# Kernel optimization log

Measured on AMD Instinct MI355X. Metric: run time of the kernel, lower is better.

The kernel has to match this reference:

```python
import jax, jax.numpy as jnp
import numpy as np

N_NODES = 100000
N_EDGES = 3200000
IN_DIM = 256
HID_DIM = 64
OUT_DIM = 64


def setup_inputs() -> dict:
    key = jax.random.key(0)
    k1, k2, k3, k4, k5, k6 = jax.random.split(key, 6)
    x = jax.random.normal(k1, (N_NODES, IN_DIM), dtype=jnp.float32)
    edge_index = jax.random.randint(k2, (2, N_EDGES), 0, N_NODES, dtype=jnp.int32)
    # Glorot-style init for the two GCNConv layers (PyG default: glorot weight, zero bias)
    W1 = jax.random.normal(k3, (IN_DIM, HID_DIM), dtype=jnp.float32) * (1.0 / np.sqrt(IN_DIM))
    b1 = jnp.zeros((HID_DIM,), dtype=jnp.float32)
    W2 = jax.random.normal(k4, (HID_DIM, OUT_DIM), dtype=jnp.float32) * (1.0 / np.sqrt(HID_DIM))
    b2 = jnp.zeros((OUT_DIM,), dtype=jnp.float32)
    return {"x": x, "edge_index": edge_index, "W1": W1, "b1": b1, "W2": W2, "b2": b2}


def _gcn_conv(x, src, dst, deg_inv_sqrt, W, b, n):
    # PyG GCNConv: h = x W; out_i = sum_j norm_ij * h_j + b, with symmetric norm
    h = x @ W                                   # (n, d_out) small GEMM
    norm = deg_inv_sqrt[src] * deg_inv_sqrt[dst]  # (E+n,)
    msg = norm[:, None] * h[src]                # gather (E+n, d_out)
    agg = jax.ops.segment_sum(msg, dst, num_segments=n)  # scatter-add
    return agg + b


def reference(x, edge_index, W1, b1, W2, b2):
    n = x.shape[0]
    loops = jnp.arange(n, dtype=edge_index.dtype)
    src = jnp.concatenate([edge_index[0], loops])
    dst = jnp.concatenate([edge_index[1], loops])
    # degree on destination (col) with added self-loops, weight 1.0
    deg = jax.ops.segment_sum(jnp.ones_like(dst, dtype=x.dtype), dst, num_segments=n)
    deg_inv_sqrt = jnp.where(deg > 0, jax.lax.rsqrt(deg), 0.0)
    h = jax.nn.relu(_gcn_conv(x, src, dst, deg_inv_sqrt, W1, b1, n))
    return _gcn_conv(h, src, dst, deg_inv_sqrt, W2, b2, n)
```

## Files before the change

kernel.cpp:

```cpp
#include <hip/hip_runtime.h>
#include <cstdint>
#include <cstddef>


#define BIN_SHIFT 7
#define BIN_NODES 128
#define MAX_BINS 1024
#define SUP_SHIFT 11
#define FINE_PER_SUP 16
#define NSUP_MAX 64
#define SCAP 56
#define SRC_BITS 17
#define SRC_MASK ((1 << SRC_BITS) - 1)

typedef unsigned short ushort_t;

typedef __attribute__((ext_vector_type(8))) short bf16x8;
typedef __attribute__((ext_vector_type(4))) float f32x4;

union FragB {
  uint4 u;
  bf16x8 b;
};

__device__ __forceinline__ float4 bfq2f4(uint2 p) {
  float4 r;
  r.x = __uint_as_float(p.x << 16);
  r.y = __uint_as_float(p.x & 0xFFFF0000u);
  r.z = __uint_as_float(p.y << 16);
  r.w = __uint_as_float(p.y & 0xFFFF0000u);
  return r;
}
__device__ __forceinline__ unsigned f2bf(float f) {
  unsigned u = __float_as_uint(f);
  return (u + 0x7FFFu + ((u >> 16) & 1u)) >> 16;
}
__device__ __forceinline__ uint2 f42bfq(float4 f) {
  uint2 r;
  r.x = f2bf(f.x) | (f2bf(f.y) << 16);
  r.y = f2bf(f.z) | (f2bf(f.w) << 16);
  return r;
}

__global__ void zero_int(int* __restrict__ p, int n) {
  int i = blockIdx.x * blockDim.x + threadIdx.x;
  if (i < n) p[i] = 0;
}

__global__ __launch_bounds__(256) void bin_count(const int* __restrict__ dst, int E, int nbins,
                                                 int* __restrict__ binCnt) {
  __shared__ int h[MAX_BINS];
  for (int i = threadIdx.x; i < nbins; i += 256) h[i] = 0;
  __syncthreads();
  int stride = gridDim.x * 256;
  for (int e = blockIdx.x * 256 + threadIdx.x; e < E; e += stride)
    atomicAdd(&h[dst[e] >> BIN_SHIFT], 1);
  __syncthreads();
  for (int i = threadIdx.x; i < nbins; i += 256)
    if (h[i]) atomicAdd(&binCnt[i], h[i]);
}

__global__ __launch_bounds__(256) void bin_scan(const int* __restrict__ binCnt, int nbins, int E,
                                                int* __restrict__ binStart,
                                                int* __restrict__ binCursor,
                                                int* __restrict__ supCursor) {
  __shared__ int s[256];
  int t = threadIdx.x;
  int c[4];
  int sum = 0;
#pragma unroll
  for (int i = 0; i < 4; i++) {
    int idx = t * 4 + i;
    c[i] = (idx < nbins) ? binCnt[idx] : 0;
    sum += c[i];
  }
  int v = sum;
  s[t] = v;
  __syncthreads();
  for (int d = 1; d < 256; d <<= 1) {
    int add = (t >= d) ? s[t - d] : 0;
    __syncthreads();
    s[t] += add;
    __syncthreads();
  }
  int run = s[t] - v;
#pragma unroll
  for (int i = 0; i < 4; i++) {
    int idx = t * 4 + i;
    if (idx < nbins) {
      binStart[idx] = run;
      binCursor[idx] = run;
      if ((idx & (FINE_PER_SUP - 1)) == 0) supCursor[idx >> 4] = run;
      run += c[i];
    }
  }
  if (t == 0) binStart[nbins] = E;
}

__global__ __launch_bounds__(256) void super_fill(const int* __restrict__ src,
                                                  const int* __restrict__ dst, int E, int nsup,
                                                  int* __restrict__ supCursor,
                                                  unsigned* __restrict__ supbuf) {
  __shared__ unsigned stage[NSUP_MAX * SCAP];
  __shared__ int lcnt[NSUP_MAX], lbase[NSUP_MAX], lscan[NSUP_MAX + 1];
  const int tid = threadIdx.x;
  const int t0 = blockIdx.x * 2048;
  const int t1 = min(E, t0 + 2048);

  int dv[8], sv[8];
#pragma unroll
  for (int i = 0; i < 8; i++) {
    int e = t0 + i * 256 + tid;
    if (e < t1) {
      dv[i] = dst[e];
      sv[i] = src[e];
    }
  }
  if (tid < nsup) lcnt[tid] = 0;
  __syncthreads();
#pragma unroll
  for (int i = 0; i < 8; i++) {
    int e = t0 + i * 256 + tid;
    if (e < t1) {
      int d = dv[i];
      int sb = d >> SUP_SHIFT;
      unsigned v = ((unsigned)(d & ((1 << SUP_SHIFT) - 1)) << SRC_BITS) | (unsigned)sv[i];
      int idx = atomicAdd(&lcnt[sb], 1);
      if (idx < SCAP)
        stage[sb * SCAP + idx] = v;
      else {
        int g = atomicAdd(&supCursor[sb], 1);
        supbuf[g] = v;
      }
    }
  }
  __syncthreads();
  if (tid < nsup) {
    int c = min(lcnt[tid], SCAP);
    lcnt[tid] = c;
    lbase[tid] = c ? atomicAdd(&supCursor[tid], c) : 0;
  }
  __syncthreads();
  if (tid < 64) {
    int vv = (tid < nsup) ? lcnt[tid] : 0;
    int ss = vv;
#pragma unroll
    for (int d = 1; d < 64; d <<= 1) {
      int u = __shfl_up(ss, d);
      if (tid >= d) ss += u;
    }
    lscan[tid + 1] = ss;
    if (tid == 0) lscan[0] = 0;
  }
  __syncthreads();
  int total = lscan[nsup];
  for (int j = tid; j < total; j += 256) {
    int lo = 0, hi = nsup;
    while (hi - lo > 1) {
      int mid = (lo + hi) >> 1;
      if (lscan[mid] <= j)
        lo = mid;
      else
        hi = mid;
    }
    int off = j - lscan[lo];
    supbuf[lbase[lo] + off] = stage[lo * SCAP + off];
  }
}

__global__ __launch_bounds__(256) void fine_fill(const unsigned* __restrict__ supbuf,
                                                 const int* __restrict__ binStart, int nbins,
                                                 int* __restrict__ binCursor,
                                                 unsigned* __restrict__ binbuf) {
  __shared__ int lcnt[FINE_PER_SUP], lbase[FINE_PER_SUP];
  int sb = blockIdx.x >> 3, p = blockIdx.x & 7;
  int seg0 = binStart[sb << 4];
  int seg1 = binStart[min((sb + 1) << 4, nbins)];
  int part = (seg1 - seg0 + 7) >> 3;
  int c0 = seg0 + p * part;
  int c1 = min(seg1, c0 + part);
  if (threadIdx.x < FINE_PER_SUP) lcnt[threadIdx.x] = 0;
  __syncthreads();
  for (int i = c0 + threadIdx.x; i < c1; i += 256) atomicAdd(&lcnt[supbuf[i] >> 24], 1);
  __syncthreads();
  if (threadIdx.x < FINE_PER_SUP) {
    int c = lcnt[threadIdx.x];
    lbase[threadIdx.x] = c ? atomicAdd(&binCursor[(sb << 4) + threadIdx.x], c) : 0;
    lcnt[threadIdx.x] = 0;
  }
  __syncthreads();
  for (int i = c0 + threadIdx.x; i < c1; i += 256) {
    unsigned v = supbuf[i];
    unsigned dls = v >> SRC_BITS;
    int f = dls >> BIN_SHIFT;
    unsigned vf = ((dls & (BIN_NODES - 1)) << SRC_BITS) | (v & SRC_MASK);
    int idx = lbase[f] + atomicAdd(&lcnt[f], 1);
    binbuf[idx] = vf;
  }
}

__global__ __launch_bounds__(256) void node_count_dis(const unsigned* __restrict__ binbuf,
                                                      const int* __restrict__ binStart, int N,
                                                      int* __restrict__ count,
                                                      float* __restrict__ dis) {
  __shared__ int cnt[BIN_NODES];
  int b = blockIdx.x;
  int nodeBase = b << BIN_SHIFT;
  if (threadIdx.x < BIN_NODES) cnt[threadIdx.x] = 0;
  __syncthreads();
  int s0 = binStart[b], s1 = binStart[b + 1];
  for (int i = s0 + threadIdx.x; i < s1; i += 256) atomicAdd(&cnt[binbuf[i] >> SRC_BITS], 1);
  __syncthreads();
  if (threadIdx.x < BIN_NODES) {
    int node = nodeBase + threadIdx.x;
    if (node < N) {
      int c = cnt[threadIdx.x];
      count[node] = c;
      dis[node] = rsqrtf((float)(c + 1));
    }
  }
}

__global__ __launch_bounds__(256) void bin_csr(const unsigned* __restrict__ binbuf,
                                               const int* __restrict__ binStart,
                                               const int* __restrict__ count, int N, int E,
                                               int* __restrict__ rowptr, int* __restrict__ col) {
  __shared__ int cur[BIN_NODES];
  __shared__ int pref[BIN_NODES];
  int b = blockIdx.x, t = threadIdx.x;
  int nodeBase = b << BIN_SHIFT;
  int c = 0;
  if (t < BIN_NODES) {
    int node = nodeBase + t;
    c = (node < N) ? count[node] : 0;
    pref[t] = c;
  }
  __syncthreads();
  for (int d = 1; d < BIN_NODES; d <<= 1) {
    int add = (t < BIN_NODES && t >= d) ? pref[t - d] : 0;
    __syncthreads();
    if (t < BIN_NODES) pref[t] += add;
    __syncthreads();
  }
  int s0 = binStart[b];
  if (t < BIN_NODES) {
    int node = nodeBase + t;
    if (node < N) {
      int ex = s0 + pref[t] - c;
      rowptr[node] = ex;
      cur[t] = ex;
    }
  }
  if (b == 0 && t == 255) rowptr[N] = E;
  __syncthreads();
  int s1 = binStart[b + 1];
  for (int i = s0 + t; i < s1; i += 256) {
    unsigned v = binbuf[i];
    int slot = atomicAdd(&cur[v >> SRC_BITS], 1);
    col[slot] = v & SRC_MASK;
  }
}

__global__ __launch_bounds__(256) void wsplit(const float* __restrict__ W1,
                                              const float* __restrict__ W2,
                                              ushort_t* __restrict__ wt1,
                                              ushort_t* __restrict__ wt2) {
  int i = blockIdx.x * 256 + threadIdx.x;
  const float* W;
  ushort_t* wt;
  int K, idx;
  if (i < 256 * 64) {
    W = W1; wt = wt1; K = 256; idx = i;
  } else if (i < 256 * 64 + 64 * 64) {
    W = W2; wt = wt2; K = 64; idx = i - 256 * 64;
  } else
    return;
  int n = idx & 63, k = idx >> 6;
  float f = W[k * 64 + n];
  unsigned u = __float_as_uint(f);
  unsigned hb = u & 0xFFFF0000u;
  float lo = f - __uint_as_float(hb);
  wt[(size_t)n * K + k] = (ushort_t)(u >> 16);
  wt[(size_t)64 * K + (size_t)n * K + k] = (ushort_t)(__float_as_uint(lo) >> 16);
}

__device__ __forceinline__ void split8u(uint4 a, uint4 b, uint4& xh, uint4& xl) {
  unsigned ua[8] = {a.x, a.y, a.z, a.w, b.x, b.y, b.z, b.w};
  unsigned hw[4], lw[4];
#pragma unroll
  for (int p = 0; p < 4; p++) {
    unsigned u0 = ua[2 * p], u1 = ua[2 * p + 1];
    unsigned h0 = u0 & 0xFFFF0000u, h1 = u1 & 0xFFFF0000u;
    float l0 = __uint_as_float(u0) - __uint_as_float(h0);
    float l1 = __uint_as_float(u1) - __uint_as_float(h1);
    hw[p] = (u0 >> 16) | h1;
    lw[p] = (__float_as_uint(l0) >> 16) | (__float_as_uint(l1) & 0xFFFF0000u);
  }
  xh = make_uint4(hw[0], hw[1], hw[2], hw[3]);
  xl = make_uint4(lw[0], lw[1], lw[2], lw[3]);
}

__global__ __launch_bounds__(256, 3) void gemm1_mfma(const float* __restrict__ A,
                                                     const ushort_t* __restrict__ Wt,
                                                     uint2* __restrict__ Cb, int M) {
  constexpr int K = 256;
  __shared__ uint4 xtile[3][4][256];
  const int lane = threadIdx.x & 63;
  const int wv = threadIdx.x >> 6;
  const int l15 = lane & 15;
  const int lq = lane >> 4;
  const int m0 = blockIdx.x * 128 + wv * 32;

  const ushort_t* __restrict__ Wlo = Wt + (size_t)64 * K;

  f32x4 acc[2][4];
#pragma unroll
  for (int a = 0; a < 2; a++)
#pragma unroll
    for (int b = 0; b < 4; b++) acc[a][b] = (f32x4){0.f, 0.f, 0.f, 0.f};

  auto stage_tile = [&](int kt, int buf) {
#pragma unroll
    for (int c = 0; c < 4; c++) {
      int s = c * 64 + lane;
      int r = s >> 3;
      int c4 = (s & 7) ^ (r & 7);
      int nd = m0 + r;
      if (nd >= M) nd = M - 1;
      const float* gp = A + (size_t)nd * K + kt * 32 + c4 * 4;
      __builtin_amdgcn_global_load_lds(
          (const __attribute__((address_space(1))) void*)gp,
          (__attribute__((address_space(3))) void*)&xtile[buf][wv][c * 64], 16, 0, 0);
    }
  };

  stage_tile(0, 0);
  stage_tile(1, 1);
  __builtin_amdgcn_sched_barrier(0);

#pragma unroll
  for (int j = 0; j < 8; j++) {
    if (j < 7)
      asm volatile("s_waitcnt vmcnt(4)" ::: "memory");
    else
      asm volatile("s_waitcnt vmcnt(0)" ::: "memory");
    __builtin_amdgcn_sched_barrier(0);
    FragB w[8];
    {
      const int kb = j * 32 + lq * 8;
#pragma unroll
      for (int nt = 0; nt < 4; nt++) {
        w[nt].u = *(const uint4*)(Wt + (size_t)(nt * 16 + l15) * K + kb);
        w[4 + nt].u = *(const uint4*)(Wlo + (size_t)(nt * 16 + l15) * K + kb);
      }
    }
    uint4 xa[2][2];
#pragma unroll
    for (int mt = 0; mt < 2; mt++) {
      int mr = mt * 16 + l15;
#pragma unroll
      for (int hh = 0; hh < 2; hh++) {
        int c4 = (lq * 2 + hh) ^ (mr & 7);
        xa[mt][hh] = *(const uint4*)&xtile[j % 3][wv][mr * 8 + c4];
      }
    }
    __builtin_amdgcn_sched_barrier(0);
    if (j + 2 < 8) stage_tile(j + 2, (j + 2) % 3);
    __builtin_amdgcn_sched_barrier(0);
    FragB xh0, xl0, xh1, xl1;
    split8u(xa[0][0], xa[0][1], xh0.u, xl0.u);
    split8u(xa[1][0], xa[1][1], xh1.u, xl1.u);
#pragma unroll
    for (int nt = 0; nt < 4; nt++) {
      acc[0][nt] = __builtin_amdgcn_mfma_f32_16x16x32_bf16(w[nt].b, xh0.b, acc[0][nt], 0, 0, 0);
      acc[0][nt] = __builtin_amdgcn_mfma_f32_16x16x32_bf16(w[nt].b, xl0.b, acc[0][nt], 0, 0, 0);
      acc[1][nt] = __builtin_amdgcn_mfma_f32_16x16x32_bf16(w[nt].b, xh1.b, acc[1][nt], 0, 0, 0);
      acc[1][nt] = __builtin_amdgcn_mfma_f32_16x16x32_bf16(w[nt].b, xl1.b, acc[1][nt], 0, 0, 0);
    }
#pragma unroll
    for (int nt = 0; nt < 4; nt++) {
      acc[0][nt] = __builtin_amdgcn_mfma_f32_16x16x32_bf16(w[4 + nt].b, xh0.b, acc[0][nt], 0, 0, 0);
      acc[1][nt] = __builtin_amdgcn_mfma_f32_16x16x32_bf16(w[4 + nt].b, xh1.b, acc[1][nt], 0, 0, 0);
    }
  }

#pragma unroll
  for (int mt = 0; mt < 2; mt++) {
    int node = m0 + mt * 16 + l15;
    if (node < M) {
      uint2* cp = Cb + (size_t)node * 16 + lq;
#pragma unroll
      for (int nt = 0; nt < 4; nt++) {
        float4 o = make_float4(acc[mt][nt][0], acc[mt][nt][1], acc[mt][nt][2], acc[mt][nt][3]);
        cp[nt * 4] = f42bfq(o);
      }
    }
  }
}

__global__ __launch_bounds__(256, 3) void gemm2_mfma(const ushort_t* __restrict__ Av,
                                                     const ushort_t* __restrict__ Wt,
                                                     uint2* __restrict__ Cb, int M) {
  constexpr int K = 64;
  constexpr int NT = K / 32;
  const int lane = threadIdx.x & 63;
  const int wv = threadIdx.x >> 6;
  const int l15 = lane & 15;
  const int lq = lane >> 4;
  const int m0 = blockIdx.x * 128 + wv * 32;

  const ushort_t* __restrict__ Wlo = Wt + (size_t)64 * K;

  f32x4 acc[2][4];
#pragma unroll
  for (int a = 0; a < 2; a++)
#pragma unroll
    for (int b = 0; b < 4; b++) acc[a][b] = (f32x4){0.f, 0.f, 0.f, 0.f};

  int node[2], ncl[2];
#pragma unroll
  for (int mt = 0; mt < 2; mt++) {
    node[mt] = m0 + mt * 16 + l15;
    ncl[mt] = node[mt] < M ? node[mt] : (M - 1);
  }

  FragB xa[NT][2], wh[NT][4], wl[NT][4];
#pragma unroll
  for (int t = 0; t < NT; t++)
#pragma unroll
    for (int mt = 0; mt < 2; mt++)
      xa[t][mt].u = *(const uint4*)(Av + (size_t)ncl[mt] * K + t * 32 + lq * 8);
#pragma unroll
  for (int t = 0; t < NT; t++)
#pragma unroll
    for (int nt = 0; nt < 4; nt++) {
      wh[t][nt].u = *(const uint4*)(Wt + (size_t)(nt * 16 + l15) * K + t * 32 + lq * 8);
      wl[t][nt].u = *(const uint4*)(Wlo + (size_t)(nt * 16 + l15) * K + t * 32 + lq * 8);
    }
#pragma unroll
  for (int t = 0; t < NT; t++)
#pragma unroll
    for (int mt = 0; mt < 2; mt++)
#pragma unroll
      for (int nt = 0; nt < 4; nt++) {
        acc[mt][nt] =
            __builtin_amdgcn_mfma_f32_16x16x32_bf16(wh[t][nt].b, xa[t][mt].b, acc[mt][nt], 0, 0, 0);
        acc[mt][nt] =
            __builtin_amdgcn_mfma_f32_16x16x32_bf16(wl[t][nt].b, xa[t][mt].b, acc[mt][nt], 0, 0, 0);
      }

#pragma unroll
  for (int mt = 0; mt < 2; mt++) {
    if (node[mt] < M) {
      uint2* cp = Cb + (size_t)node[mt] * 16 + lq;
#pragma unroll
      for (int nt = 0; nt < 4; nt++) {
        float4 o = make_float4(acc[mt][nt][0], acc[mt][nt][1], acc[mt][nt][2], acc[mt][nt][3]);
        cp[nt * 4] = f42bfq(o);
      }
    }
  }
}

template <bool OUTBF>
__global__ __launch_bounds__(256) void agg_kernel(
    const uint2* __restrict__ h, const int* __restrict__ rowptr, const int* __restrict__ col,
    const float* __restrict__ dis, const float* __restrict__ bias, void* __restrict__ outv,
    int N, int relu) {
  int wq = (blockIdx.x * blockDim.x + threadIdx.x) >> 6;
  int n0 = wq * 4;
  if (n0 >= N) return;
  int lane = threadIdx.x & 63;
  int sub = lane & 15;
  int quarter = lane >> 4;

  int rp[5];
  float dd[4];
#pragma unroll
  for (int i = 0; i < 5; i++) rp[i] = rowptr[min(n0 + i, N)];
#pragma unroll
  for (int i = 0; i < 4; i++) dd[i] = (n0 + i < N) ? dis[n0 + i] : 0.f;
  float4 bv = ((const float4*)bias)[sub];

#pragma unroll
  for (int ni = 0; ni < 4; ni++) {
    int wid = n0 + ni;
    if (wid >= N) break;
    int start = rp[ni], end = rp[ni + 1];
    float di = dd[ni];

    float4 a0 = make_float4(0.f, 0.f, 0.f, 0.f), a1 = a0, a2 = a0, a3 = a0;
    {
      float4 self = bfq2f4(h[(size_t)wid * 16 + sub]);
      if (quarter == 0) {
        a0.x = di * self.x;
        a0.y = di * self.y;
        a0.z = di * self.z;
        a0.w = di * self.w;
      }
    }

    for (int base = start; base < end; base += 64) {
      int e = base + lane;
      int sj = 0;
      float wj = 0.f;
      if (e < end) {
        sj = col[e];
        wj = dis[sj];
      }
      int cnt = end - base;
      if (cnt > 64) cnt = 64;
      int rounds = (cnt + 3) >> 2;
      int t = 0;
      for (; t + 4 <= rounds; t += 4) {
        int i0 = 4 * t + quarter;
        int s0 = __shfl(sj, i0), s1 = __shfl(sj, i0 + 4), s2 = __shfl(sj, i0 + 8),
            s3 = __shfl(sj, i0 + 12);
        float w0 = __shfl(wj, i0), w1 = __shfl(wj, i0 + 4), w2 = __shfl(wj, i0 + 8),
              w3 = __shfl(wj, i0 + 12);
        float4 g0 = bfq2f4(h[(size_t)s0 * 16 + sub]);
        float4 g1 = bfq2f4(h[(size_t)s1 * 16 + sub]);
        float4 g2 = bfq2f4(h[(size_t)s2 * 16 + sub]);
        float4 g3 = bfq2f4(h[(size_t)s3 * 16 + sub]);
        a0.x += w0 * g0.x; a0.y += w0 * g0.y; a0.z += w0 * g0.z; a0.w += w0 * g0.w;
        a1.x += w1 * g1.x; a1.y += w1 * g1.y; a1.z += w1 * g1.z; a1.w += w1 * g1.w;
        a2.x += w2 * g2.x; a2.y += w2 * g2.y; a2.z += w2 * g2.z; a2.w += w2 * g2.w;
        a3.x += w3 * g3.x; a3.y += w3 * g3.y; a3.z += w3 * g3.z; a3.w += w3 * g3.w;
      }
      for (; t < rounds; t++) {
        int i0 = 4 * t + quarter;
        int s0 = __shfl(sj, i0);
        float w0 = __shfl(wj, i0);
        float4 g0 = bfq2f4(h[(size_t)s0 * 16 + sub]);
        a0.x += w0 * g0.x; a0.y += w0 * g0.y; a0.z += w0 * g0.z; a0.w += w0 * g0.w;
      }
    }

    float sx = (a0.x + a1.x) + (a2.x + a3.x);
    float sy = (a0.y + a1.y) + (a2.y + a3.y);
    float sz = (a0.z + a1.z) + (a2.z + a3.z);
    float sw = (a0.w + a1.w) + (a2.w + a3.w);
    sx += __shfl_down(sx, 32); sy += __shfl_down(sy, 32);
    sz += __shfl_down(sz, 32); sw += __shfl_down(sw, 32);
    sx += __shfl_down(sx, 16); sy += __shfl_down(sy, 16);
    sz += __shfl_down(sz, 16); sw += __shfl_down(sw, 16);
    if (quarter == 0) {
      float4 o = make_float4(di * sx + bv.x, di * sy + bv.y, di * sz + bv.z, di * sw + bv.w);
      if (relu) {
        o.x = fmaxf(o.x, 0.f);
        o.y = fmaxf(o.y, 0.f);
        o.z = fmaxf(o.z, 0.f);
        o.w = fmaxf(o.w, 0.f);
      }
      if (OUTBF)
        ((uint2*)outv)[(size_t)wid * 16 + sub] = f42bfq(o);
      else
        ((float4*)outv)[(size_t)wid * 16 + sub] = o;
    }
  }
}

extern "C" void kernel_launch(void* const* d_in, const int* in_sizes, int n_in,
                              void* d_out, int out_size, void* d_ws, size_t ws_size,
                              hipStream_t stream) {
  const float* x = (const float*)d_in[0];
  const int* ei = (const int*)d_in[1];
  const float* W1 = (const float*)d_in[2];
  const float* b1 = (const float*)d_in[3];
  const float* W2 = (const float*)d_in[4];
  const float* b2 = (const float*)d_in[5];

  const int IN = 256;
  const int E = in_sizes[1] / 2;
  const int N = in_sizes[0] / IN;
  const int* src = ei;
  const int* dst = ei + E;
  const int nbins = (N + BIN_NODES - 1) >> BIN_SHIFT;
  const int nsup = (N + (1 << SUP_SHIFT) - 1) >> SUP_SHIFT;

  char* ws = (char*)d_ws;
  size_t off = 0;
  auto alloc = [&](size_t bytes) -> void* {
    void* p = ws + off;
    off += (bytes + 255) & ~(size_t)255;
    return p;
  };
  int* count = (int*)alloc((size_t)N * 4);
  int* rowptr = (int*)alloc((size_t)(N + 1) * 4);
  float* dis = (float*)alloc((size_t)N * 4);
  int* binCnt = (int*)alloc(MAX_BINS * 4);
  int* binStart = (int*)alloc((MAX_BINS + 1) * 4);
  int* binCursor = (int*)alloc(MAX_BINS * 4);
  int* supCursor = (int*)alloc(NSUP_MAX * 4);
  int* col = (int*)alloc((size_t)E * 4);
  unsigned* supbuf = (unsigned*)col;
  uint2* out1 = (uint2*)alloc((size_t)N * 64 * 2);
  size_t big = ((size_t)E * 4 > (size_t)N * 128) ? (size_t)E * 4 : (size_t)N * 128;
  unsigned* binbuf = (unsigned*)alloc(big);
  uint2* h = (uint2*)binbuf;
  ushort_t* wt1 = (ushort_t*)alloc((size_t)2 * 64 * 256 * 2);
  ushort_t* wt2 = (ushort_t*)alloc((size_t)2 * 64 * 64 * 2);
  float* outf = (float*)d_out;

  zero_int<<<(nbins + 255) / 256, 256, 0, stream>>>(binCnt, nbins);
  bin_count<<<1024, 256, 0, stream>>>(dst, E, nbins, binCnt);
  bin_scan<<<1, 256, 0, stream>>>(binCnt, nbins, E, binStart, binCursor, supCursor);
  super_fill<<<(E + 2047) / 2048, 256, 0, stream>>>(src, dst, E, nsup, supCursor, supbuf);
  fine_fill<<<nsup * 8, 256, 0, stream>>>(supbuf, binStart, nbins, binCursor, binbuf);
  node_count_dis<<<nbins, 256, 0, stream>>>(binbuf, binStart, N, count, dis);
  bin_csr<<<nbins, 256, 0, stream>>>(binbuf, binStart, count, N, E, rowptr, col);
  wsplit<<<(256 * 64 + 64 * 64 + 255) / 256, 256, 0, stream>>>(W1, W2, wt1, wt2);

  gemm1_mfma<<<(N + 127) / 128, 256, 0, stream>>>(x, wt1, h, N);
  agg_kernel<true><<<(N + 15) / 16, 256, 0, stream>>>(h, rowptr, col, dis, b1, out1, N, 1);
  gemm2_mfma<<<(N + 127) / 128, 256, 0, stream>>>((const ushort_t*)out1, wt2, h, N);
  agg_kernel<false><<<(N + 15) / 16, 256, 0, stream>>>(h, rowptr, col, dis, b2, outf, N, 0);
}
```

Baseline: 473.2 us.

## Software-pipeline gathers in aggregation, one node per wave, reorder GEMM waitcnt

```diff
diff --git a/kernel.cpp b/kernel.cpp
--- a/kernel.cpp
+++ b/kernel.cpp
@@ -340,11 +340,6 @@
 
 #pragma unroll
   for (int j = 0; j < 8; j++) {
-    if (j < 7)
-      asm volatile("s_waitcnt vmcnt(4)" ::: "memory");
-    else
-      asm volatile("s_waitcnt vmcnt(0)" ::: "memory");
-    __builtin_amdgcn_sched_barrier(0);
     FragB w[8];
     {
       const int kb = j * 32 + lq * 8;
@@ -354,6 +349,12 @@
         w[4 + nt].u = *(const uint4*)(Wlo + (size_t)(nt * 16 + l15) * K + kb);
       }
     }
+    __builtin_amdgcn_sched_barrier(0);
+    if (j < 7)
+      asm volatile("s_waitcnt vmcnt(12)" ::: "memory");
+    else
+      asm volatile("s_waitcnt vmcnt(8)" ::: "memory");
+    __builtin_amdgcn_sched_barrier(0);
     uint4 xa[2][2];
 #pragma unroll
     for (int mt = 0; mt < 2; mt++) {
@@ -467,96 +468,105 @@
     const uint2* __restrict__ h, const int* __restrict__ rowptr, const int* __restrict__ col,
     const float* __restrict__ dis, const float* __restrict__ bias, void* __restrict__ outv,
     int N, int relu) {
-  int wq = (blockIdx.x * blockDim.x + threadIdx.x) >> 6;
-  int n0 = wq * 4;
-  if (n0 >= N) return;
+  int wid = (blockIdx.x * blockDim.x + threadIdx.x) >> 6;
+  if (wid >= N) return;
   int lane = threadIdx.x & 63;
   int sub = lane & 15;
   int quarter = lane >> 4;
 
-  int rp[5];
-  float dd[4];
-#pragma unroll
-  for (int i = 0; i < 5; i++) rp[i] = rowptr[min(n0 + i, N)];
-#pragma unroll
-  for (int i = 0; i < 4; i++) dd[i] = (n0 + i < N) ? dis[n0 + i] : 0.f;
-  float4 bv = ((const float4*)bias)[sub];
-
-#pragma unroll
-  for (int ni = 0; ni < 4; ni++) {
-    int wid = n0 + ni;
-    if (wid >= N) break;
-    int start = rp[ni], end = rp[ni + 1];
-    float di = dd[ni];
-
-    float4 a0 = make_float4(0.f, 0.f, 0.f, 0.f), a1 = a0, a2 = a0, a3 = a0;
-    {
-      float4 self = bfq2f4(h[(size_t)wid * 16 + sub]);
-      if (quarter == 0) {
-        a0.x = di * self.x;
-        a0.y = di * self.y;
-        a0.z = di * self.z;
-        a0.w = di * self.w;
-      }
-    }
-
-    for (int base = start; base < end; base += 64) {
-      int e = base + lane;
-      int sj = 0;
-      float wj = 0.f;
-      if (e < end) {
-        sj = col[e];
-        wj = dis[sj];
-      }
-      int cnt = end - base;
-      if (cnt > 64) cnt = 64;
-      int rounds = (cnt + 3) >> 2;
-      int t = 0;
-      for (; t + 4 <= rounds; t += 4) {
-        int i0 = 4 * t + quarter;
-        int s0 = __shfl(sj, i0), s1 = __shfl(sj, i0 + 4), s2 = __shfl(sj, i0 + 8),
-            s3 = __shfl(sj, i0 + 12);
-        float w0 = __shfl(wj, i0), w1 = __shfl(wj, i0 + 4), w2 = __shfl(wj, i0 + 8),
-              w3 = __shfl(wj, i0 + 12);
-        float4 g0 = bfq2f4(h[(size_t)s0 * 16 + sub]);
-        float4 g1 = bfq2f4(h[(size_t)s1 * 16 + sub]);
-        float4 g2 = bfq2f4(h[(size_t)s2 * 16 + sub]);
-        float4 g3 = bfq2f4(h[(size_t)s3 * 16 + sub]);
-        a0.x += w0 * g0.x; a0.y += w0 * g0.y; a0.z += w0 * g0.z; a0.w += w0 * g0.w;
-        a1.x += w1 * g1.x; a1.y += w1 * g1.y; a1.z += w1 * g1.z; a1.w += w1 * g1.w;
-        a2.x += w2 * g2.x; a2.y += w2 * g2.y; a2.z += w2 * g2.z; a2.w += w2 * g2.w;
-        a3.x += w3 * g3.x; a3.y += w3 * g3.y; a3.z += w3 * g3.z; a3.w += w3 * g3.w;
-      }
-      for (; t < rounds; t++) {
-        int i0 = 4 * t + quarter;
-        int s0 = __shfl(sj, i0);
-        float w0 = __shfl(wj, i0);
-        float4 g0 = bfq2f4(h[(size_t)s0 * 16 + sub]);
-        a0.x += w0 * g0.x; a0.y += w0 * g0.y; a0.z += w0 * g0.z; a0.w += w0 * g0.w;
-      }
-    }
-
-    float sx = (a0.x + a1.x) + (a2.x + a3.x);
-    float sy = (a0.y + a1.y) + (a2.y + a3.y);
-    float sz = (a0.z + a1.z) + (a2.z + a3.z);
-    float sw = (a0.w + a1.w) + (a2.w + a3.w);
-    sx += __shfl_down(sx, 32); sy += __shfl_down(sy, 32);
-    sz += __shfl_down(sz, 32); sw += __shfl_down(sw, 32);
-    sx += __shfl_down(sx, 16); sy += __shfl_down(sy, 16);
-    sz += __shfl_down(sz, 16); sw += __shfl_down(sw, 16);
+  int start = rowptr[wid], end = rowptr[wid + 1];
+  float di = dis[wid];
+
+  float4 a0 = make_float4(0.f, 0.f, 0.f, 0.f), a1 = a0, a2 = a0, a3 = a0;
+  {
+    float4 self = bfq2f4(h[(size_t)wid * 16 + sub]);
     if (quarter == 0) {
-      float4 o = make_float4(di * sx + bv.x, di * sy + bv.y, di * sz + bv.z, di * sw + bv.w);
-      if (relu) {
-        o.x = fmaxf(o.x, 0.f);
-        o.y = fmaxf(o.y, 0.f);
-        o.z = fmaxf(o.z, 0.f);
-        o.w = fmaxf(o.w, 0.f);
-      }
-      if (OUTBF)
-        ((uint2*)outv)[(size_t)wid * 16 + sub] = f42bfq(o);
-      else
-        ((float4*)outv)[(size_t)wid * 16 + sub] = o;
-    }
+      a0.x = di * self.x;
+      a0.y = di * self.y;
+      a0.z = di * self.z;
+      a0.w = di * self.w;
+    }
+  }
+
+  for (int base = start; base < end; base += 64) {
+    int e = base + lane;
+    int sj = 0;
+    float wj = 0.f;
+    if (e < end) {
+      sj = col[e];
+      wj = dis[sj];
+    }
+    int cnt = end - base;
+    if (cnt > 64) cnt = 64;
+    int rounds = (cnt + 3) >> 2;
+
+    uint2 g0, g1, g2, g3;
+    float w0, w1, w2, w3;
+#define ISSUE(gi, G, W)                                              \
+  do {                                                               \
+    int _i = (4 * (gi) + quarter) & 63;                              \
+    int _s = __shfl(sj, _i);                                         \
+    float _w = __shfl(wj, _i);                                       \
+    if ((gi) < rounds) {                                             \
+      G = h[(size_t)_s * 16 + sub];                                  \
+      W = _w;                                                        \
+    } else {                                                         \
+      G = make_uint2(0u, 0u);                                        \
+      W = 0.f;                                                       \
+    }                                                                \
+  } while (0)
+
+    ISSUE(0, g0, w0);
+    ISSUE(1, g1, w1);
+    ISSUE(2, g2, w2);
+    ISSUE(3, g3, w3);
+    int rounds4 = (rounds + 3) & ~3;
+    for (int t0 = 0; t0 < rounds4; t0 += 4) {
+      {
+        float4 gf = bfq2f4(g0);
+        a0.x += w0 * gf.x; a0.y += w0 * gf.y; a0.z += w0 * gf.z; a0.w += w0 * gf.w;
+      }
+      ISSUE(t0 + 4, g0, w0);
+      {
+        float4 gf = bfq2f4(g1);
+        a1.x += w1 * gf.x; a1.y += w1 * gf.y; a1.z += w1 * gf.z; a1.w += w1 * gf.w;
+      }
+      ISSUE(t0 + 5, g1, w1);
+      {
+        float4 gf = bfq2f4(g2);
+        a2.x += w2 * gf.x; a2.y += w2 * gf.y; a2.z += w2 * gf.z; a2.w += w2 * gf.w;
+      }
+      ISSUE(t0 + 6, g2, w2);
+      {
+        float4 gf = bfq2f4(g3);
+        a3.x += w3 * gf.x; a3.y += w3 * gf.y; a3.z += w3 * gf.z; a3.w += w3 * gf.w;
+      }
+      ISSUE(t0 + 7, g3, w3);
+    }
+#undef ISSUE
+  }
+
+  float sx = (a0.x + a1.x) + (a2.x + a3.x);
+  float sy = (a0.y + a1.y) + (a2.y + a3.y);
+  float sz = (a0.z + a1.z) + (a2.z + a3.z);
+  float sw = (a0.w + a1.w) + (a2.w + a3.w);
+  sx += __shfl_down(sx, 32); sy += __shfl_down(sy, 32);
+  sz += __shfl_down(sz, 32); sw += __shfl_down(sw, 32);
+  sx += __shfl_down(sx, 16); sy += __shfl_down(sy, 16);
+  sz += __shfl_down(sz, 16); sw += __shfl_down(sw, 16);
+  if (quarter == 0) {
+    float4 bv = ((const float4*)bias)[sub];
+    float4 o = make_float4(di * sx + bv.x, di * sy + bv.y, di * sz + bv.z, di * sw + bv.w);
+    if (relu) {
+      o.x = fmaxf(o.x, 0.f);
+      o.y = fmaxf(o.y, 0.f);
+      o.z = fmaxf(o.z, 0.f);
+      o.w = fmaxf(o.w, 0.f);
+    }
+    if (OUTBF)
+      ((uint2*)outv)[(size_t)wid * 16 + sub] = f42bfq(o);
+    else
+      ((float4*)outv)[(size_t)wid * 16 + sub] = o;
   }
 }
 
@@ -612,7 +622,7 @@
   wsplit<<<(256 * 64 + 64 * 64 + 255) / 256, 256, 0, stream>>>(W1, W2, wt1, wt2);
 
   gemm1_mfma<<<(N + 127) / 128, 256, 0, stream>>>(x, wt1, h, N);
-  agg_kernel<true><<<(N + 15) / 16, 256, 0, stream>>>(h, rowptr, col, dis, b1, out1, N, 1);
+  agg_kernel<true><<<(N + 3) / 4, 256, 0, stream>>>(h, rowptr, col, dis, b1, out1, N, 1);
   gemm2_mfma<<<(N + 127) / 128, 256, 0, stream>>>((const ushort_t*)out1, wt2, h, N);
-  agg_kernel<false><<<(N + 15) / 16, 256, 0, stream>>>(h, rowptr, col, dis, b2, outf, N, 0);
-}
+  agg_kernel<false><<<(N + 3) / 4, 256, 0, stream>>>(h, rowptr, col, dis, b2, outf, N, 0);
+}
```

Result: faster. 461.3 us (-2.5%).
